# Kernel tuning notes

Hardware: AMD Instinct MI355X
Metric: run time of the kernel (lower is better)

The kernel has to match this reference:

```python
import jax, jax.numpy as jnp
import numpy as np

N_ROWS = 200_000   # output dim (len(distances))
N_COLS = 200_000   # input dim
NNZ = N_ROWS * 64  # avg 64 neighbors per unitig


def setup_inputs() -> dict:
    key = jax.random.key(0)
    k1, k2, k3, k4, k5 = jax.random.split(key, 5)
    rows = jnp.sort(jax.random.randint(k1, (NNZ,), 0, N_ROWS))  # COO row ids, sorted
    cols = jax.random.randint(k2, (NNZ,), 0, N_COLS)            # COO col ids
    vals = jax.random.normal(k3, (NNZ,), dtype=jnp.float32)     # sparse weight values
    x = jax.random.normal(k4, (N_COLS, 1), dtype=jnp.float32)   # dense input column vector
    bias = jax.random.normal(k5, (N_ROWS,), dtype=jnp.float32)
    return {"vals": vals, "x": x, "bias": bias, "rows": rows, "cols": cols, "n_rows": N_ROWS}


def reference(vals, x, bias, rows, cols, n_rows):
    # y = sparse.mm(W, x).squeeze(1) + bias, W in COO form (rows, cols, vals)
    gathered = vals * x[cols, 0]                      # [nnz]
    y = jax.ops.segment_sum(gathered, rows, num_segments=n_rows,
                            indices_are_sorted=True)  # [n_rows]
    return y + bias
```

## Files before the change

### kernel.cpp

```cpp
#include <hip/hip_runtime.h>


constexpr int CHUNK = 8;

__global__ void init_y_bias(const float* __restrict__ bias,
                            float* __restrict__ y, int n) {
    int i = blockIdx.x * blockDim.x + threadIdx.x;
    if (i < n) y[i] = bias[i];
}

__global__ __launch_bounds__(256) void spmv_coo_seg(
        const float* __restrict__ vals,
        const float* __restrict__ x,
        const int*   __restrict__ rows,
        const int*   __restrict__ cols,
        float*       __restrict__ y,
        long long nnz) {
    long long t  = (long long)blockIdx.x * blockDim.x + threadIdx.x;
    long long i0 = t * CHUNK;
    if (i0 >= nnz) return;

    if (i0 + CHUNK <= nnz) {
        const float4* v4 = reinterpret_cast<const float4*>(vals + i0);
        const int4*   r4 = reinterpret_cast<const int4*>(rows + i0);
        const int4*   c4 = reinterpret_cast<const int4*>(cols + i0);
        float4 va = v4[0], vb = v4[1];
        int4   ra = r4[0], rb = r4[1];
        int4   ca = c4[0], cb = c4[1];

        float v[CHUNK] = {va.x, va.y, va.z, va.w, vb.x, vb.y, vb.z, vb.w};
        int   r[CHUNK] = {ra.x, ra.y, ra.z, ra.w, rb.x, rb.y, rb.z, rb.w};
        int   c[CHUNK] = {ca.x, ca.y, ca.z, ca.w, cb.x, cb.y, cb.z, cb.w};

        float g[CHUNK];
        #pragma unroll
        for (int k = 0; k < CHUNK; ++k) g[k] = x[c[k]];

        float sum = 0.f;
        int   cur = r[0];
        #pragma unroll
        for (int k = 0; k < CHUNK; ++k) {
            if (r[k] != cur) {
                atomicAdd(&y[cur], sum);
                sum = 0.f;
                cur = r[k];
            }
            sum += v[k] * g[k];
        }
        atomicAdd(&y[cur], sum);
    } else {
        float sum = 0.f;
        int   cur = rows[i0];
        for (long long k = i0; k < nnz; ++k) {
            int rk = rows[k];
            if (rk != cur) {
                atomicAdd(&y[cur], sum);
                sum = 0.f;
                cur = rk;
            }
            sum += vals[k] * x[cols[k]];
        }
        atomicAdd(&y[cur], sum);
    }
}

extern "C" void kernel_launch(void* const* d_in, const int* in_sizes, int n_in,
                              void* d_out, int out_size, void* d_ws, size_t ws_size,
                              hipStream_t stream) {
    const float* vals = (const float*)d_in[0];
    const float* x    = (const float*)d_in[1];
    const float* bias = (const float*)d_in[2];
    const int*   rows = (const int*)d_in[3];
    const int*   cols = (const int*)d_in[4];
    float* y = (float*)d_out;

    const long long nnz = in_sizes[0];
    const int n_rows    = in_sizes[2];

    {
        int threads = 256;
        int blocks  = (n_rows + threads - 1) / threads;
        init_y_bias<<<blocks, threads, 0, stream>>>(bias, y, n_rows);
    }

    {
        long long n_thr = (nnz + CHUNK - 1) / CHUNK;
        int threads = 256;
        long long blocks = (n_thr + threads - 1) / threads;
        spmv_coo_seg<<<(int)blocks, threads, 0, stream>>>(vals, x, rows, cols, y, nnz);
    }
}
```

Measured before the change: 240.8 us.

## Replace per-segment atomics with wavefront segmented scan and direct stores

Adds a wavefront-level segmented scan using shuffles so that rows lying entirely inside a wavefront are reduced in registers and written once with a plain store of bias plus sum. Atomics remain only for rows that touch the first or last row of the wavefront. The aim is to cut atomic traffic, since each row of about 64 nonzeros was previously split across about 8 threads that each issued an atomic. The cost is extra shuffle instructions, plus the init kernel still writing bias to rows that are later overwritten.

```diff
diff --git a/kernel.cpp b/kernel.cpp
--- a/kernel.cpp
+++ b/kernel.cpp
@@ -9,58 +9,100 @@
     if (i < n) y[i] = bias[i];
 }
 
-__global__ __launch_bounds__(256) void spmv_coo_seg(
+__global__ __launch_bounds__(256) void spmv_coo_segscan(
         const float* __restrict__ vals,
         const float* __restrict__ x,
         const int*   __restrict__ rows,
         const int*   __restrict__ cols,
+        const float* __restrict__ bias,
         float*       __restrict__ y,
         long long nnz) {
     long long t  = (long long)blockIdx.x * blockDim.x + threadIdx.x;
     long long i0 = t * CHUNK;
-    if (i0 >= nnz) return;
+    int lane = threadIdx.x & 63;
 
-    if (i0 + CHUNK <= nnz) {
-        const float4* v4 = reinterpret_cast<const float4*>(vals + i0);
-        const int4*   r4 = reinterpret_cast<const int4*>(rows + i0);
-        const int4*   c4 = reinterpret_cast<const int4*>(cols + i0);
-        float4 va = v4[0], vb = v4[1];
-        int4   ra = r4[0], rb = r4[1];
-        int4   ca = c4[0], cb = c4[1];
+    long long wave_start = (t - lane) * (long long)CHUNK;
+    bool wave_full = (wave_start + 64LL * CHUNK) <= nnz;
 
-        float v[CHUNK] = {va.x, va.y, va.z, va.w, vb.x, vb.y, vb.z, vb.w};
-        int   r[CHUNK] = {ra.x, ra.y, ra.z, ra.w, rb.x, rb.y, rb.z, rb.w};
-        int   c[CHUNK] = {ca.x, ca.y, ca.z, ca.w, cb.x, cb.y, cb.z, cb.w};
-
-        float g[CHUNK];
-        #pragma unroll
-        for (int k = 0; k < CHUNK; ++k) g[k] = x[c[k]];
-
+    if (!wave_full) {
+        if (i0 >= nnz) return;
         float sum = 0.f;
-        int   cur = r[0];
-        #pragma unroll
-        for (int k = 0; k < CHUNK; ++k) {
-            if (r[k] != cur) {
-                atomicAdd(&y[cur], sum);
-                sum = 0.f;
-                cur = r[k];
-            }
-            sum += v[k] * g[k];
-        }
-        atomicAdd(&y[cur], sum);
-    } else {
-        float sum = 0.f;
-        int   cur = rows[i0];
-        for (long long k = i0; k < nnz; ++k) {
+        int cur = rows[i0];
+        long long end = i0 + CHUNK < nnz ? i0 + CHUNK : nnz;
+        for (long long k = i0; k < end; ++k) {
             int rk = rows[k];
-            if (rk != cur) {
-                atomicAdd(&y[cur], sum);
-                sum = 0.f;
-                cur = rk;
-            }
+            if (rk != cur) { atomicAdd(&y[cur], sum); sum = 0.f; cur = rk; }
             sum += vals[k] * x[cols[k]];
         }
         atomicAdd(&y[cur], sum);
+        return;
+    }
+
+    const float4* v4 = reinterpret_cast<const float4*>(vals + i0);
+    const int4*   r4 = reinterpret_cast<const int4*>(rows + i0);
+    const int4*   c4 = reinterpret_cast<const int4*>(cols + i0);
+    float4 va = v4[0], vb = v4[1];
+    int4   ra = r4[0], rb = r4[1];
+    int4   ca = c4[0], cb = c4[1];
+
+    float v[CHUNK] = {va.x, va.y, va.z, va.w, vb.x, vb.y, vb.z, vb.w};
+    int   r[CHUNK] = {ra.x, ra.y, ra.z, ra.w, rb.x, rb.y, rb.z, rb.w};
+    int   c[CHUNK] = {ca.x, ca.y, ca.z, ca.w, cb.x, cb.y, cb.z, cb.w};
+
+    float g[CHUNK];
+    #pragma unroll
+    for (int k = 0; k < CHUNK; ++k) g[k] = x[c[k]];
+
+    int   first_row = r[0];
+    int   cur = first_row;
+    float sum = v[0] * g[0];
+    bool  head_done = false;
+    int   head_row = 0;
+    float head_sum = 0.f;
+    #pragma unroll
+    for (int k = 1; k < CHUNK; ++k) {
+        if (r[k] != cur) {
+            if (!head_done) { head_done = true; head_row = cur; head_sum = sum; }
+            else {
+                y[cur] = bias[cur] + sum;
+            }
+            cur = r[k];
+            sum = 0.f;
+        }
+        sum += v[k] * g[k];
+    }
+    int   tail_row = cur;
+    float tail_sum = sum;
+
+    float scan = tail_sum;
+    #pragma unroll
+    for (int off = 1; off < 64; off <<= 1) {
+        int   orow = __shfl_up(tail_row, off);
+        float osum = __shfl_up(scan, off);
+        if (lane >= off && orow == tail_row) scan += osum;
+    }
+
+    int   prev_tail_row  = __shfl_up(tail_row, 1);
+    float prev_scan      = __shfl_up(scan, 1);
+    int   next_first     = __shfl_down(first_row, 1);
+    int   wave_first_row = __shfl(first_row, 0);
+    int   wave_last_row  = __shfl(tail_row, 63);
+
+    if (head_done) {
+        float total = head_sum;
+        if (lane > 0 && prev_tail_row == head_row) total += prev_scan;
+        if (head_row == wave_first_row)
+            atomicAdd(&y[head_row], total);
+        else
+            y[head_row] = bias[head_row] + total;
+    }
+
+    bool tail_end = (lane == 63) || (next_first != tail_row);
+    if (tail_end) {
+        if (tail_row == wave_first_row || tail_row == wave_last_row)
+            atomicAdd(&y[tail_row], scan);
+        else
+            y[tail_row] = bias[tail_row] + scan;
     }
 }
 
@@ -87,6 +129,7 @@
         long long n_thr = (nnz + CHUNK - 1) / CHUNK;
         int threads = 256;
         long long blocks = (n_thr + threads - 1) / threads;
-        spmv_coo_seg<<<(int)blocks, threads, 0, stream>>>(vals, x, rows, cols, y, nnz);
+        spmv_coo_segscan<<<(int)blocks, threads, 0, stream>>>(
+            vals, x, rows, cols, bias, y, nnz);
     }
 }
```

Result: slower. 279.4 us (+16.0%).

## Accumulate per-block row sums in LDS and write interior rows directly

Applied to the files above, without the earlier changes.

Each block now owns a contiguous 4096-element span of sorted COO entries and accumulates partial row sums into a shared-memory array indexed relative to the block's first row. Interior rows are written straight to y with the bias added, and only the two boundary rows go through global atomics. This cuts most global atomic traffic. CHUNK grows to 16 and the streaming loads become nontemporal. The cost is an LDS zero-init pass, two barriers, and a fallback path when a span covers more rows than the shared buffer holds.

```diff
diff --git a/kernel.cpp b/kernel.cpp
--- a/kernel.cpp
+++ b/kernel.cpp
@@ -1,7 +1,13 @@
 #include <hip/hip_runtime.h>
 
 
-constexpr int CHUNK = 8;
+constexpr int       CHUNK = 16;
+constexpr int       BLOCK = 256;
+constexpr long long SPAN  = (long long)BLOCK * CHUNK;
+constexpr int       RMAX  = 6144;
+
+typedef float vfloat4 __attribute__((ext_vector_type(4)));
+typedef int   vint4   __attribute__((ext_vector_type(4)));
 
 __global__ void init_y_bias(const float* __restrict__ bias,
                             float* __restrict__ y, int n) {
@@ -9,58 +15,103 @@
     if (i < n) y[i] = bias[i];
 }
 
-__global__ __launch_bounds__(256) void spmv_coo_seg(
+__device__ __forceinline__ void lds_add(float* p, float v) {
+    __hip_atomic_fetch_add(p, v, __ATOMIC_RELAXED, __HIP_MEMORY_SCOPE_WORKGROUP);
+}
+
+__global__ __launch_bounds__(BLOCK) void spmv_coo_lds(
         const float* __restrict__ vals,
         const float* __restrict__ x,
         const int*   __restrict__ rows,
         const int*   __restrict__ cols,
+        const float* __restrict__ bias,
         float*       __restrict__ y,
         long long nnz) {
-    long long t  = (long long)blockIdx.x * blockDim.x + threadIdx.x;
-    long long i0 = t * CHUNK;
-    if (i0 >= nnz) return;
+    __shared__ float acc[RMAX];
+    const int tid = threadIdx.x;
+    const long long b0 = (long long)blockIdx.x * SPAN;
+    if (b0 >= nnz) return;
+    const long long bend = (b0 + SPAN < nnz) ? (b0 + SPAN) : nnz;
 
-    if (i0 + CHUNK <= nnz) {
-        const float4* v4 = reinterpret_cast<const float4*>(vals + i0);
-        const int4*   r4 = reinterpret_cast<const int4*>(rows + i0);
-        const int4*   c4 = reinterpret_cast<const int4*>(cols + i0);
-        float4 va = v4[0], vb = v4[1];
-        int4   ra = r4[0], rb = r4[1];
-        int4   ca = c4[0], cb = c4[1];
+    const int r0    = rows[b0];
+    const int rl    = rows[bend - 1];
+    const int range = rl - r0 + 1;
 
-        float v[CHUNK] = {va.x, va.y, va.z, va.w, vb.x, vb.y, vb.z, vb.w};
-        int   r[CHUNK] = {ra.x, ra.y, ra.z, ra.w, rb.x, rb.y, rb.z, rb.w};
-        int   c[CHUNK] = {ca.x, ca.y, ca.z, ca.w, cb.x, cb.y, cb.z, cb.w};
+    if (range <= RMAX) {
+        for (int i = tid; i < range; i += BLOCK) acc[i] = 0.f;
+        __syncthreads();
 
-        float g[CHUNK];
-        #pragma unroll
-        for (int k = 0; k < CHUNK; ++k) g[k] = x[c[k]];
+        const long long i0 = b0 + (long long)tid * CHUNK;
+        if (i0 < bend) {
+            if (i0 + CHUNK <= bend) {
+                const vfloat4* v4 = reinterpret_cast<const vfloat4*>(vals + i0);
+                const vint4*   r4 = reinterpret_cast<const vint4*>(rows + i0);
+                const vint4*   c4 = reinterpret_cast<const vint4*>(cols + i0);
+                float v[CHUNK]; int r[CHUNK]; int c[CHUNK];
+                #pragma unroll
+                for (int q = 0; q < CHUNK / 4; ++q) {
+                    vfloat4 vv = __builtin_nontemporal_load(v4 + q);
+                    vint4   rr = __builtin_nontemporal_load(r4 + q);
+                    vint4   cc = __builtin_nontemporal_load(c4 + q);
+                    #pragma unroll
+                    for (int j = 0; j < 4; ++j) {
+                        v[4*q+j] = vv[j];
+                        r[4*q+j] = rr[j];
+                        c[4*q+j] = cc[j];
+                    }
+                }
+                float g[CHUNK];
+                #pragma unroll
+                for (int k = 0; k < CHUNK; ++k) g[k] = x[c[k]];
 
-        float sum = 0.f;
-        int   cur = r[0];
-        #pragma unroll
-        for (int k = 0; k < CHUNK; ++k) {
-            if (r[k] != cur) {
-                atomicAdd(&y[cur], sum);
-                sum = 0.f;
-                cur = r[k];
+                int   cur = r[0];
+                float sum = v[0] * g[0];
+                #pragma unroll
+                for (int k = 1; k < CHUNK; ++k) {
+                    if (r[k] != cur) {
+                        lds_add(&acc[cur - r0], sum);
+                        cur = r[k];
+                        sum = 0.f;
+                    }
+                    sum += v[k] * g[k];
+                }
+                lds_add(&acc[cur - r0], sum);
+            } else {
+                int   cur = rows[i0];
+                float sum = 0.f;
+                long long kend = (i0 + CHUNK < bend) ? (i0 + CHUNK) : bend;
+                for (long long k = i0; k < kend; ++k) {
+                    int rk = rows[k];
+                    if (rk != cur) { lds_add(&acc[cur - r0], sum); sum = 0.f; cur = rk; }
+                    sum += vals[k] * x[cols[k]];
+                }
+                lds_add(&acc[cur - r0], sum);
             }
-            sum += v[k] * g[k];
         }
-        atomicAdd(&y[cur], sum);
+        __syncthreads();
+
+        for (int i = tid; i < range; i += BLOCK) {
+            int   r = r0 + i;
+            float a = acc[i];
+            if (r == r0 || r == rl) {
+                if (a != 0.f) atomicAdd(&y[r], a);
+            } else {
+                y[r] = bias[r] + a;
+            }
+        }
     } else {
-        float sum = 0.f;
-        int   cur = rows[i0];
-        for (long long k = i0; k < nnz; ++k) {
-            int rk = rows[k];
-            if (rk != cur) {
-                atomicAdd(&y[cur], sum);
-                sum = 0.f;
-                cur = rk;
+        const long long i0 = b0 + (long long)tid * CHUNK;
+        if (i0 < bend) {
+            int   cur = rows[i0];
+            float sum = 0.f;
+            long long kend = (i0 + CHUNK < bend) ? (i0 + CHUNK) : bend;
+            for (long long k = i0; k < kend; ++k) {
+                int rk = rows[k];
+                if (rk != cur) { atomicAdd(&y[cur], sum); sum = 0.f; cur = rk; }
+                sum += vals[k] * x[cols[k]];
             }
-            sum += vals[k] * x[cols[k]];
+            atomicAdd(&y[cur], sum);
         }
-        atomicAdd(&y[cur], sum);
     }
 }
 
@@ -84,9 +135,8 @@
     }
 
     {
-        long long n_thr = (nnz + CHUNK - 1) / CHUNK;
-        int threads = 256;
-        long long blocks = (n_thr + threads - 1) / threads;
-        spmv_coo_seg<<<(int)blocks, threads, 0, stream>>>(vals, x, rows, cols, y, nnz);
+        long long blocks = (nnz + SPAN - 1) / SPAN;
+        spmv_coo_lds<<<(int)blocks, BLOCK, 0, stream>>>(
+            vals, x, rows, cols, bias, y, nnz);
     }
 }
```

Measured after the change: 218.1 us. 9.5% less time.
